# Kernel tuning notes

Measured on AMD Instinct MI355X. Metric: run time of the kernel, lower is better.

## Reference

```python
import jax, jax.numpy as jnp
import numpy as np

DECAY = 0.99
EPS = 1e-05


def setup_inputs() -> dict:
    key = jax.random.key(0)
    k1, k2, k3, k4 = jax.random.split(key, 4)
    x = jax.random.normal(k1, (32, 64, 64, 64), jnp.float32)          # [B,H,W,dim]
    embed = jax.random.normal(k2, (64, 1024), jnp.float32)            # [dim, n_embed] buffer
    cluster_size = jax.random.uniform(k3, (1024,), jnp.float32)       # EMA cluster-size buffer
    embed_avg = jax.random.normal(k4, (64, 1024), jnp.float32)        # EMA embed-avg buffer
    return {"x": x, "embed": embed, "cluster_size": cluster_size, "embed_avg": embed_avg}


def reference(x, embed, cluster_size, embed_avg):
    dim = x.shape[-1]
    n_embed = embed.shape[1]
    flatten = x.reshape(-1, dim)                                      # [N, dim]
    # squared distances: ||f||^2 - 2 f.E + ||e||^2   -> [N, n_embed]
    dist = ((flatten * flatten).sum(1, keepdims=True)
            - 2.0 * (flatten @ embed)
            + (embed * embed).sum(0, keepdims=True))
    idx = jnp.argmin(dist, axis=1)                                    # [N]
    quantize = jnp.take(embed.T, idx, axis=0).reshape(x.shape)        # codebook gather
    embed_ind = idx.reshape(x.shape[:-1])

    # EMA codebook update (training branch); stats detached as in torch (buffers, .data ops)
    fl = jax.lax.stop_gradient(flatten)
    onehot_sum = jax.ops.segment_sum(jnp.ones_like(idx, dtype=x.dtype), idx, num_segments=n_embed)
    embed_sum = jax.ops.segment_sum(fl, idx, num_segments=n_embed).T  # [dim, n_embed]
    new_cluster_size = DECAY * cluster_size + (1.0 - DECAY) * onehot_sum
    new_embed_avg = DECAY * embed_avg + (1.0 - DECAY) * embed_sum
    n = new_cluster_size.sum()
    cs = (new_cluster_size + EPS) / (n + n_embed * EPS) * n
    new_embed = new_embed_avg / cs[None, :]

    diff = jnp.mean((jax.lax.stop_gradient(quantize) - x) ** 2)       # commitment loss
    quantize_st = x + jax.lax.stop_gradient(quantize - x)             # straight-through
    return (quantize_st, diff, embed_ind, new_cluster_size, new_embed_avg, new_embed)
```

## Files before the change

kernel.cpp:

```cpp
#include <hip/hip_runtime.h>


#define N_ROWS 131072
#define DIM    64
#define NEMB   1024
#define FLAG_CAP 131072
#define TAU 0.02f
#define NRANGE 32

static constexpr float DECAYF = 0.99f;
static constexpr float OMDF   = (float)(1.0 - 0.99);
static constexpr float EPSF   = 1e-5f;
static constexpr float NEPSF  = (float)(1024 * 1e-5);

typedef __attribute__((ext_vector_type(8))) short short8;
typedef __attribute__((ext_vector_type(4))) float f32x4;

static __device__ __forceinline__ unsigned short f2bf(float f) {
    unsigned int u = __builtin_bit_cast(unsigned int, f);
    unsigned int r = (u + 0x7FFFu + ((u >> 16) & 1u)) >> 16;
    return (unsigned short)r;
}
static __device__ __forceinline__ float bf2f(unsigned short h) {
    unsigned int u = ((unsigned int)h) << 16;
    return __builtin_bit_cast(float, u);
}

static __device__ __forceinline__ void glds16(const uint4* g, uint4* l) {
    __builtin_amdgcn_global_load_lds(
        (const __attribute__((address_space(1))) unsigned int*)(g),
        (__attribute__((address_space(3))) unsigned int*)(l), 16, 0, 0);
}

#define WS_ESUM    0
#define WS_CNTF    65536
#define WS_DIFF    66560
#define WS_FLAGCNT 66561
#define WS_N       66562
#define WS_EE      66564
#define WS_EMBEDT  67588
#define WS_IDX     133124
#define WS_FLAGLST 264196
#define WS_BFRAG   395268
#define WS_CNTPART 460804
#define WS_PART    493572
#define WS_NEED_BYTES ((size_t)(WS_PART + NRANGE * 65536) * 4)

__global__ void prep_kernel(const float* __restrict__ embed,
                            float* __restrict__ embedT,
                            float* __restrict__ ee,
                            uint4* __restrict__ BfragG) {
    int tid = blockIdx.x * 256 + threadIdx.x;
    for (int i = 0; i < 4; ++i) {
        int id = i * 16384 + tid;
        int d = id >> 10, e = id & 1023;
        embedT[e * 64 + d] = embed[id];
    }
    if (tid < NEMB) {
        float s = 0.f;
        for (int d = 0; d < DIM; ++d) {
            float v = embed[d * 1024 + tid];
            s = fmaf(v, v, s);
        }
        ee[tid] = s;
    }
    int fid  = tid >> 6;
    int lane = tid & 63;
    int hl = fid & 1, kt = (fid >> 1) & 1, ct = fid >> 2;
    int col = ct * 16 + (lane & 15);
    int k0  = kt * 32 + (lane >> 4) * 8;
    unsigned short u[8];
    #pragma unroll
    for (int j = 0; j < 8; ++j) {
        float v = -2.0f * embed[(k0 + j) * 1024 + col];
        unsigned short h = f2bf(v);
        if (hl) h = f2bf(v - bf2f(h));
        u[j] = h;
    }
    uint4 wv;
    wv.x = (unsigned)u[0] | ((unsigned)u[1] << 16);
    wv.y = (unsigned)u[2] | ((unsigned)u[3] << 16);
    wv.z = (unsigned)u[4] | ((unsigned)u[5] << 16);
    wv.w = (unsigned)u[6] | ((unsigned)u[7] << 16);
    BfragG[fid * 64 + lane] = wv;
}

__global__ __launch_bounds__(256) void dist_kernel(
        const float* __restrict__ x, const uint4* __restrict__ BfragG,
        const float* __restrict__ ee, const float* __restrict__ embedT,
        float* __restrict__ out_q, float* __restrict__ out_ind,
        int* __restrict__ ws_idx, float* __restrict__ ws_diff,
        int* __restrict__ ws_flagcnt, int* __restrict__ ws_flaglist) {
    __shared__ uint4 Bs[2][1024];
    __shared__ float sEE[1024];
    __shared__ int   sIdx[128];
    __shared__ float red[4];

    const int t = threadIdx.x;
    const int w = t >> 6, lane = t & 63;
    const int quad = lane >> 4, wl = lane & 15;
    const int rbase = blockIdx.x * 128;

    short8 a_hi[2][2], a_lo[2][2];
    #pragma unroll
    for (int rt = 0; rt < 2; ++rt) {
        int row = rbase + w * 32 + rt * 16 + wl;
        #pragma unroll
        for (int kt = 0; kt < 2; ++kt) {
            const float* px = x + (size_t)row * 64 + kt * 32 + quad * 8;
            float4 v0 = *(const float4*)px;
            float4 v1 = *(const float4*)(px + 4);
            float vv[8] = {v0.x, v0.y, v0.z, v0.w, v1.x, v1.y, v1.z, v1.w};
            short8 ah, al;
            #pragma unroll
            for (int j = 0; j < 8; ++j) {
                unsigned short h = f2bf(vv[j]);
                ah[j] = (short)h;
                al[j] = (short)f2bf(vv[j] - bf2f(h));
            }
            a_hi[rt][kt] = ah; a_lo[rt][kt] = al;
        }
    }

    for (int i = t; i < 1024; i += 256) sEE[i] = ee[i];

    float b1[8], b2[8];
    int   i1[8];
    #pragma unroll
    for (int s = 0; s < 8; ++s) { b1[s] = 3.4e38f; b2[s] = 3.4e38f; i1[s] = 0; }

    const f32x4 zacc = {0.f, 0.f, 0.f, 0.f};

    __syncthreads();

#define STAGE(chv, bv)                                                     \
    {                                                                      \
        const uint4* _src = BfragG + (chv) * 1024 + w * 256 + lane;        \
        uint4* _dst = &Bs[bv][w * 256];                                    \
        glds16(_src,       _dst);                                          \
        glds16(_src + 64,  _dst + 64);                                     \
        glds16(_src + 128, _dst + 128);                                    \
        glds16(_src + 192, _dst + 192);                                    \
    }

    int buf = 0;
    STAGE(0, 0);
    for (int ch = 0; ch < 16; ++ch) {
        if (ch < 15) {
            STAGE(ch + 1, buf ^ 1);
            asm volatile("s_waitcnt vmcnt(4)" ::: "memory");
        } else {
            asm volatile("s_waitcnt vmcnt(0)" ::: "memory");
        }
        __builtin_amdgcn_s_barrier();
        asm volatile("" ::: "memory");

        const short8* bp = (const short8*)&Bs[buf][0];
        #pragma unroll
        for (int ctl = 0; ctl < 4; ++ctl) {
            short8 bh0 = bp[(ctl * 4 + 0) * 64 + lane];
            short8 bl0 = bp[(ctl * 4 + 1) * 64 + lane];
            short8 bh1 = bp[(ctl * 4 + 2) * 64 + lane];
            short8 bl1 = bp[(ctl * 4 + 3) * 64 + lane];
            int col = ch * 64 + ctl * 16 + wl;
            float eec = sEE[col];
            #pragma unroll
            for (int rt = 0; rt < 2; ++rt) {
                f32x4 c0 = __builtin_amdgcn_mfma_f32_16x16x32_bf16(a_lo[rt][0], bh0, zacc, 0, 0, 0);
                f32x4 c1 = __builtin_amdgcn_mfma_f32_16x16x32_bf16(a_lo[rt][1], bh1, zacc, 0, 0, 0);
                c0 = __builtin_amdgcn_mfma_f32_16x16x32_bf16(a_hi[rt][0], bl0, c0, 0, 0, 0);
                c1 = __builtin_amdgcn_mfma_f32_16x16x32_bf16(a_hi[rt][1], bl1, c1, 0, 0, 0);
                c0 = __builtin_amdgcn_mfma_f32_16x16x32_bf16(a_hi[rt][0], bh0, c0, 0, 0, 0);
                c1 = __builtin_amdgcn_mfma_f32_16x16x32_bf16(a_hi[rt][1], bh1, c1, 0, 0, 0);
                #pragma unroll
                for (int reg = 0; reg < 4; ++reg) {
                    float s = c0[reg] + c1[reg] + eec;
                    int st = rt * 4 + reg;
                    bool lt = s < b1[st];
                    b2[st] = fminf(fmaxf(s, b1[st]), b2[st]);
                    i1[st] = lt ? col : i1[st];
                    b1[st] = fminf(s, b1[st]);
                }
            }
        }
        asm volatile("s_waitcnt lgkmcnt(0)" ::: "memory");
        __builtin_amdgcn_s_barrier();
        buf ^= 1;
    }
#undef STAGE

    for (int m = 1; m < 16; m <<= 1) {
        #pragma unroll
        for (int s = 0; s < 8; ++s) {
            float ob1 = __shfl_xor(b1[s], m);
            int   oi1 = __shfl_xor(i1[s], m);
            float ob2 = __shfl_xor(b2[s], m);
            if (ob1 < b1[s] || (ob1 == b1[s] && oi1 < i1[s])) {
                b2[s] = fminf(b1[s], ob2); b1[s] = ob1; i1[s] = oi1;
            } else {
                b2[s] = fminf(b2[s], ob1);
            }
        }
    }
    if (wl == 0) {
        #pragma unroll
        for (int s = 0; s < 8; ++s) {
            int rt = s >> 2, reg = s & 3;
            int rloc = w * 32 + rt * 16 + quad * 4 + reg;
            int row = rbase + rloc;
            sIdx[rloc] = i1[s];
            ws_idx[row] = i1[s];
            out_ind[row] = (float)i1[s];
            if (b2[s] - b1[s] < TAU) {
                int pos = atomicAdd(ws_flagcnt, 1);
                if (pos < FLAG_CAP) ws_flaglist[pos] = row;
            }
        }
    }
    __syncthreads();

    {
        int r = t >> 1, hh = t & 1;
        int e = sIdx[r];
        const float4* et = (const float4*)(embedT + e * 64 + hh * 32);
        const float4* xr = (const float4*)(x + (size_t)(rbase + r) * 64 + hh * 32);
        float4*       qo = (float4*)(out_q + (size_t)(rbase + r) * 64 + hh * 32);
        float dsum = 0.f;
        #pragma unroll
        for (int v = 0; v < 8; ++v) {
            float4 q4 = et[v];
            float4 x4 = xr[v];
            float dx = q4.x - x4.x, dy = q4.y - x4.y, dz = q4.z - x4.z, dw = q4.w - x4.w;
            float4 o;
            o.x = x4.x + dx; o.y = x4.y + dy; o.z = x4.z + dz; o.w = x4.w + dw;
            qo[v] = o;
            dsum += dx * dx + dy * dy + dz * dz + dw * dw;
        }
        for (int o2 = 32; o2 > 0; o2 >>= 1) dsum += __shfl_down(dsum, o2);
        if (lane == 0) red[w] = dsum;
        __syncthreads();
        if (t == 0) atomicAdd(ws_diff, red[0] + red[1] + red[2] + red[3]);
    }
}

__global__ __launch_bounds__(256) void recheck_kernel(
        const float* __restrict__ x, const float* __restrict__ embed,
        const float* __restrict__ embedT, const float* __restrict__ ee,
        const int* __restrict__ flagcnt, const int* __restrict__ flaglist,
        int* __restrict__ ws_idx, float* __restrict__ out_ind,
        float* __restrict__ out_q, float* __restrict__ ws_diff) {
    __shared__ float sx[8][64];
    __shared__ float sff[8];
    __shared__ int   srow[8];
    __shared__ float sbd[8][256];
    __shared__ int   sbi[8][256];
    const int t = threadIdx.x;
    const int w = t >> 6, lane = t & 63;
    int cnt = *flagcnt;
    if (cnt > FLAG_CAP) cnt = FLAG_CAP;
    int ntiles = (cnt + 7) >> 3;
    for (int tile = blockIdx.x; tile < ntiles; tile += gridDim.x) {
        int base = tile * 8;
        int nr = cnt - base; if (nr > 8) nr = 8;
        __syncthreads();
        if (t < nr) srow[t] = flaglist[base + t];
        __syncthreads();
        for (int l = t; l < nr * 64; l += 256)
            sx[l >> 6][l & 63] = x[(size_t)srow[l >> 6] * 64 + (l & 63)];
        __syncthreads();
        if (t < nr) {
            float ff = 0.f;
            for (int k = 0; k < 64; ++k) ff = fmaf(sx[t][k], sx[t][k], ff);
            sff[t] = ff;
        }
        float acc[8][4];
        #pragma unroll
        for (int r = 0; r < 8; ++r)
            #pragma unroll
            for (int j = 0; j < 4; ++j) acc[r][j] = 0.f;
        int c0 = t * 4;
        for (int k = 0; k < 64; ++k) {
            float4 e4 = *(const float4*)(embed + k * 1024 + c0);
            #pragma unroll
            for (int r = 0; r < 8; ++r) {
                float xk = sx[r][k];
                acc[r][0] = fmaf(xk, e4.x, acc[r][0]);
                acc[r][1] = fmaf(xk, e4.y, acc[r][1]);
                acc[r][2] = fmaf(xk, e4.z, acc[r][2]);
                acc[r][3] = fmaf(xk, e4.w, acc[r][3]);
            }
        }
        __syncthreads();
        #pragma unroll
        for (int r = 0; r < 8; ++r) {
            float ff = sff[r];
            float bd = 3.4e38f; int bi = 0;
            #pragma unroll
            for (int j = 0; j < 4; ++j) {
                float d = (ff - 2.f * acc[r][j]) + ee[c0 + j];
                if (d < bd) { bd = d; bi = c0 + j; }
            }
            sbd[r][t] = bd; sbi[r][t] = bi;
        }
        __syncthreads();
        #pragma unroll
        for (int rr = 0; rr < 2; ++rr) {
            int r = w * 2 + rr;
            if (r < nr) {
                float bd = sbd[r][lane]; int bi = sbi[r][lane];
                #pragma unroll
                for (int k2 = 1; k2 < 4; ++k2) {
                    float od = sbd[r][lane + 64 * k2];
                    int   oi = sbi[r][lane + 64 * k2];
                    if (od < bd || (od == bd && oi < bi)) { bd = od; bi = oi; }
                }
                for (int m = 32; m > 0; m >>= 1) {
                    float od = __shfl_xor(bd, m);
                    int   oi = __shfl_xor(bi, m);
                    if (od < bd || (od == bd && oi < bi)) { bd = od; bi = oi; }
                }
                int row = srow[r];
                int oi_old = ws_idx[row];
                if (bi != oi_old) {
                    float xv = sx[r][lane];
                    float dn   = embedT[bi * 64 + lane] - xv;
                    float dold = embedT[oi_old * 64 + lane] - xv;
                    out_q[(size_t)row * 64 + lane] = xv + dn;
                    float delta = dn * dn - dold * dold;
                    for (int o = 32; o > 0; o >>= 1) delta += __shfl_down(delta, o);
                    if (lane == 0) {
                        ws_idx[row] = bi;
                        out_ind[row] = (float)bi;
                        atomicAdd(ws_diff, delta);
                    }
                }
            }
        }
    }
}

__global__ __launch_bounds__(256) void scatter_kernel(
        const int* __restrict__ idx, const float* __restrict__ x,
        float* __restrict__ part_or_esum, float* __restrict__ cntp_or_cntf,
        int use_atomic) {
    __shared__ float shist[8192];
    __shared__ float scnt[1024];
    const int t = threadIdx.x;
    const int rb = blockIdx.x >> 3, oct = blockIdx.x & 7;
    const int w = t >> 6, lane = t & 63;
    const int g = lane >> 3, d = lane & 7;

    for (int i = t; i < 8192; i += 256) shist[i] = 0.f;
    if (oct == 0) for (int i = t; i < 1024; i += 256) scnt[i] = 0.f;
    __syncthreads();

    const int row0 = rb * 4096 + w * 1024;
    int rcur = row0 + g;
    int e_n = idx[rcur];
    float x_n = x[(size_t)rcur * 64 + oct * 8 + d];
    for (int it = 0; it < 128; ++it) {
        int e = e_n; float xv = x_n;
        int rnext = rcur + 8;
        if (it < 127) {
            e_n = idx[rnext];
            x_n = x[(size_t)rnext * 64 + oct * 8 + d];
        }
        rcur = rnext;
        atomicAdd(&shist[d * 1024 + e], xv);
        if (oct == 0 && d == 0) atomicAdd(&scnt[e], 1.0f);
    }
    __syncthreads();

    if (!use_atomic) {
        float* dst = part_or_esum + (size_t)blockIdx.x * 8192;
        for (int cell = t; cell < 8192; cell += 256) dst[cell] = shist[cell];
        if (oct == 0) {
            float* cdst = cntp_or_cntf + rb * 1024;
            for (int i = t; i < 1024; i += 256) cdst[i] = scnt[i];
        }
    } else {
        for (int cell = t; cell < 8192; cell += 256) {
            float v = shist[cell];
            if (v != 0.f)
                atomicAdd(&part_or_esum[(oct * 8 + (cell >> 10)) * 1024 + (cell & 1023)], v);
        }
        if (oct == 0) {
            for (int i = t; i < 1024; i += 256) {
                float c = scnt[i];
                if (c != 0.f) atomicAdd(&cntp_or_cntf[i], c);
            }
        }
    }
}

__global__ __launch_bounds__(1024) void finalize1(
        const float* __restrict__ cluster_size, const float* __restrict__ cntp,
        int nrb, const float* __restrict__ ws_diff, float* __restrict__ out_diff,
        float* __restrict__ out_ncs, float* __restrict__ ws_n) {
    int t = threadIdx.x;
    float c = 0.f;
    for (int k = 0; k < nrb; ++k) c += cntp[k * 1024 + t];
    float ncs = DECAYF * cluster_size[t] + OMDF * c;
    out_ncs[t] = ncs;
    __shared__ float sred[16];
    float v = ncs;
    for (int o = 32; o > 0; o >>= 1) v += __shfl_down(v, o);
    if ((t & 63) == 0) sred[t >> 6] = v;
    __syncthreads();
    if (t == 0) {
        float n = 0.f;
        for (int i = 0; i < 16; ++i) n += sred[i];
        ws_n[0] = n;
        out_diff[0] = ws_diff[0] * (1.0f / 8388608.0f);
    }
}

__global__ __launch_bounds__(256) void finalize2(
        const float* __restrict__ embed_avg, const float* __restrict__ part,
        int nrb, const float* __restrict__ out_ncs, const float* __restrict__ ws_n,
        float* __restrict__ out_nea, float* __restrict__ out_ne) {
    int j = blockIdx.x * 256 + threadIdx.x;
    float es = 0.f;
    for (int k = 0; k < nrb; ++k) es += part[(size_t)k * 65536 + j];
    float n = ws_n[0];
    float nea = DECAYF * embed_avg[j] + OMDF * es;
    out_nea[j] = nea;
    float ncs = out_ncs[j & 1023];
    float cs = (ncs + EPSF) / (n + NEPSF) * n;
    out_ne[j] = nea / cs;
}

extern "C" void kernel_launch(void* const* d_in, const int* in_sizes, int n_in,
                              void* d_out, int out_size, void* d_ws, size_t ws_size,
                              hipStream_t stream) {
    const float* x            = (const float*)d_in[0];
    const float* embed        = (const float*)d_in[1];
    const float* cluster_size = (const float*)d_in[2];
    const float* embed_avg    = (const float*)d_in[3];

    float* out = (float*)d_out;
    float* out_q    = out;
    float* out_diff = out + 8388608;
    float* out_ind  = out + 8388609;
    float* out_ncs  = out + 8519681;
    float* out_nea  = out + 8520705;
    float* out_ne   = out + 8586241;

    float* ws = (float*)d_ws;
    float* ws_esum     = ws + WS_ESUM;
    float* ws_cntf     = ws + WS_CNTF;
    float* ws_diff     = ws + WS_DIFF;
    int*   ws_flagcnt  = (int*)(ws + WS_FLAGCNT);
    float* ws_n        = ws + WS_N;
    float* ws_ee       = ws + WS_EE;
    float* ws_embedT   = ws + WS_EMBEDT;
    int*   ws_idx      = (int*)(ws + WS_IDX);
    int*   ws_flaglist = (int*)(ws + WS_FLAGLST);
    uint4* ws_Bfrag    = (uint4*)(ws + WS_BFRAG);
    float* ws_cntpart  = ws + WS_CNTPART;
    float* ws_part     = ws + WS_PART;

    const int use_part = (ws_size >= WS_NEED_BYTES) ? 1 : 0;

    if (use_part) {
        hipMemsetAsync(ws + WS_DIFF, 0, 8, stream);
    } else {
        hipMemsetAsync(d_ws, 0, (size_t)(WS_FLAGCNT + 1) * 4, stream);
    }

    prep_kernel<<<64, 256, 0, stream>>>(embed, ws_embedT, ws_ee, ws_Bfrag);
    dist_kernel<<<N_ROWS / 128, 256, 0, stream>>>(x, ws_Bfrag, ws_ee, ws_embedT,
                                                  out_q, out_ind, ws_idx, ws_diff,
                                                  ws_flagcnt, ws_flaglist);
    recheck_kernel<<<512, 256, 0, stream>>>(x, embed, ws_embedT, ws_ee,
                                            ws_flagcnt, ws_flaglist,
                                            ws_idx, out_ind, out_q, ws_diff);
    scatter_kernel<<<NRANGE * 8, 256, 0, stream>>>(
        ws_idx, x,
        use_part ? ws_part : ws_esum,
        use_part ? ws_cntpart : ws_cntf,
        use_part ? 0 : 1);
    finalize1<<<1, 1024, 0, stream>>>(cluster_size,
                                      use_part ? ws_cntpart : ws_cntf,
                                      use_part ? NRANGE : 1,
                                      ws_diff, out_diff, out_ncs, ws_n);
    finalize2<<<256, 256, 0, stream>>>(embed_avg,
                                       use_part ? ws_part : ws_esum,
                                       use_part ? NRANGE : 1,
                                       out_ncs, ws_n, out_nea, out_ne);
}
```

Before: 286.7 us.

## Load codebook fragments directly to registers and retune scatter histogram layout

The distance kernel stops staging codebook B-fragments through double-buffered LDS with barriers. Each wave now loads its fragments straight from global memory into registers, prefetching one group ahead, which removes LDS traffic and block-wide syncs but makes every wave fetch the whole codebook from global/L2. Separately, the scatter kernel moves to 512 threads per block with half the rows per wave. It also switches its shared histogram to an entry-major layout (e*8+d), which spreads the LDS atomics across banks, and transposes the histogram on write-out.

```diff
diff --git a/kernel.cpp b/kernel.cpp
--- a/kernel.cpp
+++ b/kernel.cpp
@@ -24,12 +24,6 @@
 static __device__ __forceinline__ float bf2f(unsigned short h) {
     unsigned int u = ((unsigned int)h) << 16;
     return __builtin_bit_cast(float, u);
-}
-
-static __device__ __forceinline__ void glds16(const uint4* g, uint4* l) {
-    __builtin_amdgcn_global_load_lds(
-        (const __attribute__((address_space(1))) unsigned int*)(g),
-        (__attribute__((address_space(3))) unsigned int*)(l), 16, 0, 0);
 }
 
 #define WS_ESUM    0
@@ -91,7 +85,6 @@
         float* __restrict__ out_q, float* __restrict__ out_ind,
         int* __restrict__ ws_idx, float* __restrict__ ws_diff,
         int* __restrict__ ws_flagcnt, int* __restrict__ ws_flaglist) {
-    __shared__ uint4 Bs[2][1024];
     __shared__ float sEE[1024];
     __shared__ int   sIdx[128];
     __shared__ float red[4];
@@ -133,61 +126,39 @@
 
     __syncthreads();
 
-#define STAGE(chv, bv)                                                     \
-    {                                                                      \
-        const uint4* _src = BfragG + (chv) * 1024 + w * 256 + lane;        \
-        uint4* _dst = &Bs[bv][w * 256];                                    \
-        glds16(_src,       _dst);                                          \
-        glds16(_src + 64,  _dst + 64);                                     \
-        glds16(_src + 128, _dst + 128);                                    \
-        glds16(_src + 192, _dst + 192);                                    \
-    }
-
-    int buf = 0;
-    STAGE(0, 0);
-    for (int ch = 0; ch < 16; ++ch) {
-        if (ch < 15) {
-            STAGE(ch + 1, buf ^ 1);
-            asm volatile("s_waitcnt vmcnt(4)" ::: "memory");
-        } else {
-            asm volatile("s_waitcnt vmcnt(0)" ::: "memory");
-        }
-        __builtin_amdgcn_s_barrier();
-        asm volatile("" ::: "memory");
-
-        const short8* bp = (const short8*)&Bs[buf][0];
-        #pragma unroll
-        for (int ctl = 0; ctl < 4; ++ctl) {
-            short8 bh0 = bp[(ctl * 4 + 0) * 64 + lane];
-            short8 bl0 = bp[(ctl * 4 + 1) * 64 + lane];
-            short8 bh1 = bp[(ctl * 4 + 2) * 64 + lane];
-            short8 bl1 = bp[(ctl * 4 + 3) * 64 + lane];
-            int col = ch * 64 + ctl * 16 + wl;
-            float eec = sEE[col];
+    const uint4* bg = BfragG + lane;
+    uint4 nb0 = bg[0], nb1 = bg[64], nb2 = bg[128], nb3 = bg[192];
+    for (int g = 0; g < 64; ++g) {
+        uint4 c_b0 = nb0, c_b1 = nb1, c_b2 = nb2, c_b3 = nb3;
+        if (g < 63) {
+            const uint4* p = bg + (g + 1) * 256;
+            nb0 = p[0]; nb1 = p[64]; nb2 = p[128]; nb3 = p[192];
+        }
+        short8 bh0 = __builtin_bit_cast(short8, c_b0);
+        short8 bl0 = __builtin_bit_cast(short8, c_b1);
+        short8 bh1 = __builtin_bit_cast(short8, c_b2);
+        short8 bl1 = __builtin_bit_cast(short8, c_b3);
+        int col = g * 16 + wl;
+        float eec = sEE[col];
+        #pragma unroll
+        for (int rt = 0; rt < 2; ++rt) {
+            f32x4 c0 = __builtin_amdgcn_mfma_f32_16x16x32_bf16(a_lo[rt][0], bh0, zacc, 0, 0, 0);
+            f32x4 c1 = __builtin_amdgcn_mfma_f32_16x16x32_bf16(a_lo[rt][1], bh1, zacc, 0, 0, 0);
+            c0 = __builtin_amdgcn_mfma_f32_16x16x32_bf16(a_hi[rt][0], bl0, c0, 0, 0, 0);
+            c1 = __builtin_amdgcn_mfma_f32_16x16x32_bf16(a_hi[rt][1], bl1, c1, 0, 0, 0);
+            c0 = __builtin_amdgcn_mfma_f32_16x16x32_bf16(a_hi[rt][0], bh0, c0, 0, 0, 0);
+            c1 = __builtin_amdgcn_mfma_f32_16x16x32_bf16(a_hi[rt][1], bh1, c1, 0, 0, 0);
             #pragma unroll
-            for (int rt = 0; rt < 2; ++rt) {
-                f32x4 c0 = __builtin_amdgcn_mfma_f32_16x16x32_bf16(a_lo[rt][0], bh0, zacc, 0, 0, 0);
-                f32x4 c1 = __builtin_amdgcn_mfma_f32_16x16x32_bf16(a_lo[rt][1], bh1, zacc, 0, 0, 0);
-                c0 = __builtin_amdgcn_mfma_f32_16x16x32_bf16(a_hi[rt][0], bl0, c0, 0, 0, 0);
-                c1 = __builtin_amdgcn_mfma_f32_16x16x32_bf16(a_hi[rt][1], bl1, c1, 0, 0, 0);
-                c0 = __builtin_amdgcn_mfma_f32_16x16x32_bf16(a_hi[rt][0], bh0, c0, 0, 0, 0);
-                c1 = __builtin_amdgcn_mfma_f32_16x16x32_bf16(a_hi[rt][1], bh1, c1, 0, 0, 0);
-                #pragma unroll
-                for (int reg = 0; reg < 4; ++reg) {
-                    float s = c0[reg] + c1[reg] + eec;
-                    int st = rt * 4 + reg;
-                    bool lt = s < b1[st];
-                    b2[st] = fminf(fmaxf(s, b1[st]), b2[st]);
-                    i1[st] = lt ? col : i1[st];
-                    b1[st] = fminf(s, b1[st]);
-                }
-            }
-        }
-        asm volatile("s_waitcnt lgkmcnt(0)" ::: "memory");
-        __builtin_amdgcn_s_barrier();
-        buf ^= 1;
-    }
-#undef STAGE
+            for (int reg = 0; reg < 4; ++reg) {
+                float s = c0[reg] + c1[reg] + eec;
+                int st = rt * 4 + reg;
+                bool lt = s < b1[st];
+                b2[st] = fminf(fmaxf(s, b1[st]), b2[st]);
+                i1[st] = lt ? col : i1[st];
+                b1[st] = fminf(s, b1[st]);
+            }
+        }
+    }
 
     for (int m = 1; m < 16; m <<= 1) {
         #pragma unroll
@@ -339,7 +310,7 @@
     }
 }
 
-__global__ __launch_bounds__(256) void scatter_kernel(
+__global__ __launch_bounds__(512) void scatter_kernel(
         const int* __restrict__ idx, const float* __restrict__ x,
         float* __restrict__ part_or_esum, float* __restrict__ cntp_or_cntf,
         int use_atomic) {
@@ -350,42 +321,43 @@
     const int w = t >> 6, lane = t & 63;
     const int g = lane >> 3, d = lane & 7;
 
-    for (int i = t; i < 8192; i += 256) shist[i] = 0.f;
-    if (oct == 0) for (int i = t; i < 1024; i += 256) scnt[i] = 0.f;
+    for (int i = t; i < 8192; i += 512) shist[i] = 0.f;
+    if (oct == 0) for (int i = t; i < 1024; i += 512) scnt[i] = 0.f;
     __syncthreads();
 
-    const int row0 = rb * 4096 + w * 1024;
+    const int row0 = rb * 4096 + w * 512;
     int rcur = row0 + g;
     int e_n = idx[rcur];
     float x_n = x[(size_t)rcur * 64 + oct * 8 + d];
-    for (int it = 0; it < 128; ++it) {
+    for (int it = 0; it < 64; ++it) {
         int e = e_n; float xv = x_n;
         int rnext = rcur + 8;
-        if (it < 127) {
+        if (it < 63) {
             e_n = idx[rnext];
             x_n = x[(size_t)rnext * 64 + oct * 8 + d];
         }
         rcur = rnext;
-        atomicAdd(&shist[d * 1024 + e], xv);
+        atomicAdd(&shist[e * 8 + d], xv);
         if (oct == 0 && d == 0) atomicAdd(&scnt[e], 1.0f);
     }
     __syncthreads();
 
     if (!use_atomic) {
         float* dst = part_or_esum + (size_t)blockIdx.x * 8192;
-        for (int cell = t; cell < 8192; cell += 256) dst[cell] = shist[cell];
+        for (int out = t; out < 8192; out += 512)
+            dst[out] = shist[(out & 1023) * 8 + (out >> 10)];
         if (oct == 0) {
             float* cdst = cntp_or_cntf + rb * 1024;
-            for (int i = t; i < 1024; i += 256) cdst[i] = scnt[i];
+            for (int i = t; i < 1024; i += 512) cdst[i] = scnt[i];
         }
     } else {
-        for (int cell = t; cell < 8192; cell += 256) {
-            float v = shist[cell];
+        for (int out = t; out < 8192; out += 512) {
+            float v = shist[(out & 1023) * 8 + (out >> 10)];
             if (v != 0.f)
-                atomicAdd(&part_or_esum[(oct * 8 + (cell >> 10)) * 1024 + (cell & 1023)], v);
+                atomicAdd(&part_or_esum[(oct * 8 + (out >> 10)) * 1024 + (out & 1023)], v);
         }
         if (oct == 0) {
-            for (int i = t; i < 1024; i += 256) {
+            for (int i = t; i < 1024; i += 512) {
                 float c = scnt[i];
                 if (c != 0.f) atomicAdd(&cntp_or_cntf[i], c);
             }
@@ -475,7 +447,7 @@
     recheck_kernel<<<512, 256, 0, stream>>>(x, embed, ws_embedT, ws_ee,
                                             ws_flagcnt, ws_flaglist,
                                             ws_idx, out_ind, out_q, ws_diff);
-    scatter_kernel<<<NRANGE * 8, 256, 0, stream>>>(
+    scatter_kernel<<<NRANGE * 8, 512, 0, stream>>>(
         ws_idx, x,
         use_part ? ws_part : ws_esum,
         use_part ? ws_cntpart : ws_cntf,
```

Result: faster. 269.5 us (-6.0%).
